# Optimization experiments

Measured on AMD Instinct MI355X. Metric: run time of the kernel, lower is better.

Reference implementation:

```python
import jax, jax.numpy as jnp
from jax import lax
import numpy as np

B, L, C, PRED = 64, 512, 321, 96
PATCH, STRIDE = 16, 8
N = (L - PATCH) // STRIDE + 1 + 1  # 64 patches (after replication pad)
HID = PATCH * 2                    # expansion_factor=2
ALPHA, EPS = 0.2, 1e-5

def gelu(v):
    return jax.nn.gelu(v, approximate=False)  # torch nn.GELU default (erf)

def setup_inputs() -> dict:
    key = jax.random.key(0)
    ks = jax.random.split(key, 10)
    init = lambda k, s: (jax.random.normal(k, s) * 0.02).astype(jnp.float32)
    return dict(
        x=jax.random.normal(ks[0], (B, L, C), jnp.float32),
        rev_w=jnp.ones((C,), jnp.float32), rev_b=jnp.zeros((C,), jnp.float32),
        fc1_w=init(ks[1], (HID, PATCH)), fc1_b=jnp.zeros((HID,), jnp.float32),
        bn1_w=jnp.ones((N,), jnp.float32), bn1_b=jnp.zeros((N,), jnp.float32),
        conv_w=init(ks[2], (N, 1, 3)), conv_b=jnp.zeros((N,), jnp.float32),
        bn2_w=jnp.ones((N,), jnp.float32), bn2_b=jnp.zeros((N,), jnp.float32),
        fc2_w=init(ks[3], (PATCH, HID)), fc2_b=jnp.zeros((PATCH,), jnp.float32),
        m1_w=init(ks[4], (2 * N, N)), m1_b=jnp.zeros((2 * N,), jnp.float32),
        m2_w=init(ks[5], (N, 2 * N)), m2_b=jnp.zeros((N,), jnp.float32),
        gl_scale=jnp.full((1,), 0.1, jnp.float32),
        ln_w=jnp.ones((PATCH,), jnp.float32), ln_b=jnp.zeros((PATCH,), jnp.float32),
        seas_w=init(ks[6], (PRED, N * PATCH)), seas_b=jnp.zeros((PRED,), jnp.float32),
        tr_w=init(ks[7], (PRED, L)), tr_b=jnp.zeros((PRED,), jnp.float32),
        fus_w=init(ks[8], (PRED, 2 * PRED)), fus_b=jnp.zeros((PRED,), jnp.float32),
    )

def _batchnorm(h, w, b):
    # BatchNorm1d over channel axis N (train-mode batch stats, biased var)
    mu = h.mean((0, 2), keepdims=True)
    var = h.var((0, 2), keepdims=True)
    return (h - mu) * lax.rsqrt(var + EPS) * w[None, :, None] + b[None, :, None]

def reference(x, rev_w, rev_b, fc1_w, fc1_b, bn1_w, bn1_b, conv_w, conv_b,
              bn2_w, bn2_b, fc2_w, fc2_b, m1_w, m1_b, m2_w, m2_b, gl_scale,
              ln_w, ln_b, seas_w, seas_b, tr_w, tr_b, fus_w, fus_b):
    # --- RevIN norm (torch std is unbiased, ddof=1) ---
    mean = x.mean(1, keepdims=True)
    std = jnp.std(x, axis=1, ddof=1, keepdims=True) + EPS
    xn = (x - mean) / std * rev_w + rev_b
    # --- EMA trend/seasonal decomposition via scan ---
    xt = jnp.moveaxis(xn, 1, 0)                      # [L,B,C]
    def step(c, xi):
        t = ALPHA * xi + (1.0 - ALPHA) * c
        return t, t
    _, rest = lax.scan(step, xt[0], xt[1:])
    trend = jnp.moveaxis(jnp.concatenate([xt[:1], rest], 0), 0, 1)  # [B,L,C]
    seasonal = xn - trend
    # --- patching (replication pad right by STRIDE, unfold) ---
    s = seasonal.transpose(0, 2, 1).reshape(B * C, L)
    s = jnp.concatenate([s, jnp.broadcast_to(s[:, -1:], (B * C, STRIDE))], axis=1)
    idx = np.arange(N)[:, None] * STRIDE + np.arange(PATCH)[None, :]
    sp = s[:, idx]                                    # [B*C, N, PATCH]
    # --- IntraPatch (local): fc1 -> GELU -> BN -> depthwise conv -> GELU -> BN -> fc2 + res ---
    h = gelu(sp @ fc1_w.T + fc1_b)                    # [BC,N,HID]
    h = _batchnorm(h, bn1_w, bn1_b)
    h = lax.conv_general_dilated(h, conv_w, (1,), ((1, 1),),
                                 feature_group_count=N,
                                 dimension_numbers=('NCH', 'OIH', 'NCH'))
    h = h + conv_b[None, :, None]
    h = _batchnorm(gelu(h), bn2_w, bn2_b)
    local = h @ fc2_w.T + fc2_b + sp                  # dropout is identity (eval)
    # --- InterPatch (global): pool -> MLP -> sigmoid gate ---
    pooled = sp.mean(-1)                              # [BC,N]
    w = jax.nn.sigmoid(gelu(pooled @ m1_w.T + m1_b) @ m2_w.T + m2_b)
    glob = sp * (1.0 + gl_scale * w[..., None])
    # --- fusion 'add' + residual LayerNorm over PATCH ---
    y = sp + local + glob
    mu = y.mean(-1, keepdims=True)
    var = y.var(-1, keepdims=True)
    y = (y - mu) * lax.rsqrt(var + EPS) * ln_w + ln_b
    # --- heads ---
    s_pred = y.reshape(B * C, N * PATCH) @ seas_w.T + seas_b
    t = trend.transpose(0, 2, 1).reshape(B * C, L)
    t_pred = t @ tr_w.T + tr_b
    out = jnp.concatenate([s_pred, t_pred], -1) @ fus_w.T + fus_b
    out = out.reshape(B, C, PRED).transpose(0, 2, 1)  # [B,PRED,C]
    # --- RevIN denorm ---
    out = (out - rev_b) / rev_w
    return out * std + mean
```

## Files before the change

### kernel.cpp

```cpp
#include <hip/hip_runtime.h>
#include <hip/hip_bf16.h>
#include <math.h>

#define B_    64
#define L_    512
#define C_    321
#define PRED_ 96
#define N_    64
#define HID_  32
#define BC_   (B_*C_)
#define SROW_ 528
#define EPS_  1e-5f
#define ALPHA_ 0.2f
#define GR_   16
#define RB_   8
#define NBLK2_ (BC_/GR_)
#define NBLKH_ (BC_/8)
#define D64_  6.2771017353866808e-7f
#define STW_  548
#define UTW_  260

typedef __attribute__((ext_vector_type(8))) short bf16x8;
typedef __attribute__((ext_vector_type(4))) float f32x4;

__device__ __forceinline__ float gelu_f(float x){
  float ax = fabsf(x);
  float z  = ax * 0.70710678118654752440f;
  float t  = __builtin_amdgcn_rcpf(fmaf(0.3275911f, z, 1.0f));
  float poly = fmaf(fmaf(fmaf(fmaf(1.061405429f, t, -1.453152027f),
                   t, 1.421413741f), t, -0.284496736f), t, 0.254829592f) * t;
  float e  = __expf(-z*z);
  float erfp = fmaf(-poly, e, 1.0f);
  return fmaf(0.5f*ax, erfp, 0.5f*x);
}
__device__ __forceinline__ unsigned short bf16bits(float x){
  __hip_bfloat16 h = __float2bfloat16(x);
  return *(unsigned short*)&h;
}

__global__ __launch_bounds__(256) void k1_all(
    const float* __restrict__ x, const float* __restrict__ rev_w, const float* __restrict__ rev_b,
    const float* __restrict__ seas_w, const float* __restrict__ tr_w, const float* __restrict__ fus_w,
    const float* __restrict__ seas_b, const float* __restrict__ tr_b, const float* __restrict__ fus_b,
    float* __restrict__ s_raw, __hip_bfloat16* __restrict__ t_bf, float* __restrict__ rowpar,
    float* __restrict__ pooled,
    __hip_bfloat16* __restrict__ Wsf, __hip_bfloat16* __restrict__ Wtf,
    float* __restrict__ biasc, float* __restrict__ colsumT) {
  __shared__ float lf[8][32];
  __shared__ float psum[8][32], psq[8][32];
  __shared__ float fs[8][32];
  __shared__ float st[32*STW_];
  int tid = threadIdx.x;
  int bid = blockIdx.x;
  if (bid >= BC_/32) {
    int fb = bid - BC_/32;
    if (fb < 576) {
      int idx = fb*256 + tid;
      int j = idx / 1536, k = idx - j*1536;
      float acc = 0.f;
      if (k < 1024) {
        for (int i=0;i<96;++i) acc = fmaf(fus_w[j*192+i], seas_w[i*1024+k], acc);
        Wsf[(size_t)j*1024 + k] = __float2bfloat16(acc);
      } else {
        int l = k - 1024;
        for (int i=0;i<96;++i) acc = fmaf(fus_w[j*192+96+i], tr_w[i*512+l], acc);
        Wtf[(size_t)j*512 + l] = __float2bfloat16(acc);
      }
    } else {
      __shared__ float rowsum[96];
      if (tid < 96) {
        float s = 0.f;
        for (int l=0;l<512;++l) s += tr_w[tid*512+l];
        rowsum[tid] = s;
      }
      __syncthreads();
      if (tid < 96) {
        float acc = fus_b[tid], cs = 0.f;
        for (int i=0;i<96;++i) {
          acc = fmaf(fus_w[tid*192+i],    seas_b[i], acc);
          acc = fmaf(fus_w[tid*192+96+i], tr_b[i],   acc);
          cs  = fmaf(fus_w[tid*192+96+i], rowsum[i], cs);
        }
        biasc[tid] = acc; colsumT[tid] = cs;
      }
    }
    return;
  }
  int q = tid >> 5, r = tid & 31;
  int row0 = bid*32;
  int row = row0 + r;
  int b = row / C_, c = row - b*C_;
  const float* xp = x + (size_t)b*L_*C_ + c;
  int l0 = q*64;
  float sreg[64];
  float loc = 0.f, sum = 0.f, sq = 0.f;
  #pragma unroll
  for (int i=0;i<64;++i) {
    float v = xp[(size_t)(l0+i)*C_];
    sum += v; sq = fmaf(v,v,sq);
    loc = (q==0 && i==0) ? v : fmaf(ALPHA_, v, 0.8f*loc);
    sreg[i] = loc;
  }
  lf[q][r] = loc; psum[q][r] = sum; psq[q][r] = sq;
  __syncthreads();
  float cin = 0.f;
  for (int j=0;j<q;++j) cin = fmaf(D64_, cin, lf[j][r]);
  float S=0.f, Q=0.f;
  #pragma unroll
  for (int qq=0;qq<8;++qq){ S += psum[qq][r]; Q += psq[qq][r]; }
  float mean = S*(1.0f/512.0f);
  float var  = (Q - S*S*(1.0f/512.0f))*(1.0f/511.0f);
  var = fmaxf(var, 0.f);
  float stdv = sqrtf(var) + EPS_;
  float rwc = rev_w[c];
  float a = rwc / stdv;
  if (q==0) {
    float rbc = rev_b[c];
    float g = rbc - mean*a;
    float inva = stdv / rwc;
    ((float4*)rowpar)[row] = make_float4(a, g, mean, inva);
  }
  float prev = 0.f, f = 1.f, slast = 0.f;
  float sums8[8];
  #pragma unroll
  for (int j=0;j<8;++j) sums8[j] = 0.f;
  #pragma unroll
  for (int i=0;i<64;++i) {
    float lc = sreg[i];
    f *= 0.8f;
    float s = (q==0 && i==0) ? 0.f : fmaf(4.f, lc - prev, -f*cin);
    prev = lc;
    float sv = s * a;
    st[r*STW_ + q*64 + i] = sv;
    sums8[i>>3] += sv;
    slast = sv;
  }
  fs[q][r] = sums8[0];
  if (q==7) {
    #pragma unroll
    for (int k=0;k<8;++k) st[r*STW_ + 512 + k] = slast;
  }
  __syncthreads();
  for (int idx=tid; idx<32*130; idx+=256) {
    int rr = idx/130, g = idx - rr*130;
    float4 v = *(float4*)&st[rr*STW_ + g*4];
    *(float4*)&s_raw[(size_t)(row0+rr)*SROW_ + g*4] = v;
  }
  {
    float nf = (q < 7) ? fs[q+1][r] : 8.0f*slast;
    #pragma unroll
    for (int j=0;j<7;++j)
      pooled[(size_t)row*64 + q*8 + j] = (sums8[j] + sums8[j+1])*(1.0f/16.0f);
    pooled[(size_t)row*64 + q*8 + 7] = (sums8[7] + nf)*(1.0f/16.0f);
  }
  __syncthreads();
  unsigned* tb = (unsigned*)st;
  {
    float f2 = 1.f; unsigned lo = 0;
    #pragma unroll
    for (int i=0;i<64;++i) {
      f2 *= 0.8f;
      float tt = fmaf(f2, cin, sreg[i]) * a;
      unsigned hb = bf16bits(tt);
      if ((i&1)==0) lo = hb;
      else tb[r*UTW_ + q*32 + (i>>1)] = lo | (hb<<16);
    }
  }
  __syncthreads();
  for (int idx=tid; idx<32*64; idx+=256) {
    int rr = idx>>6, g = idx&63;
    uint4 v = *(uint4*)&tb[rr*UTW_ + g*4];
    *(uint4*)&t_bf[(size_t)(row0+rr)*512 + g*8] = v;
  }
}

__global__ __launch_bounds__(512) void k4_gate(
    const float* __restrict__ pooled,
    const float* __restrict__ m1_w, const float* __restrict__ m1_b,
    const float* __restrict__ m2_w, const float* __restrict__ m2_b,
    float* __restrict__ wl_g) {
  __shared__ __align__(16) __hip_bfloat16 buf[17408];
  int t = threadIdx.x;
  int row0 = blockIdx.x*64;
  __hip_bfloat16* A1 = buf;
  __hip_bfloat16* B1 = buf + 4608;
  __hip_bfloat16* H1 = buf;
  __hip_bfloat16* B2 = buf + 8704;
  for (int idx=t; idx<4096; idx+=512) {
    int r = idx>>6, k = idx&63;
    A1[r*72+k] = __float2bfloat16(pooled[(size_t)(row0+r)*64 + k]);
  }
  for (int idx=t; idx<8192; idx+=512) {
    int r = idx>>6, k = idx&63;
    B1[r*72+k] = __float2bfloat16(m1_w[idx]);
  }
  __syncthreads();
  int lane = t & 63, w = t >> 6;
  int fr = lane & 15, fg = lane >> 4;
  int mt = w & 3;
  int ng0 = (w>>2)*4;
  f32x4 acc1[4];
  #pragma unroll
  for (int nn=0;nn<4;++nn) acc1[nn] = (f32x4){0.f,0.f,0.f,0.f};
  #pragma unroll
  for (int ksub=0; ksub<2; ++ksub) {
    bf16x8 av = *(bf16x8*)&A1[(mt*16+fr)*72 + ksub*32 + fg*8];
    #pragma unroll
    for (int nn=0;nn<4;++nn) {
      bf16x8 bv = *(bf16x8*)&B1[((ng0+nn)*16+fr)*72 + ksub*32 + fg*8];
      acc1[nn] = __builtin_amdgcn_mfma_f32_16x16x32_bf16(av, bv, acc1[nn], 0,0,0);
    }
  }
  __syncthreads();
  #pragma unroll
  for (int nn=0;nn<4;++nn) {
    int col = (ng0+nn)*16 + fr;
    float bias = m1_b[col];
    #pragma unroll
    for (int reg=0;reg<4;++reg) {
      int row = mt*16 + fg*4 + reg;
      H1[row*136 + col] = __float2bfloat16(gelu_f(acc1[nn][reg] + bias));
    }
  }
  for (int idx=t; idx<8192; idx+=512) {
    int r = idx>>7, k = idx&127;
    B2[r*136+k] = __float2bfloat16(m2_w[idx]);
  }
  __syncthreads();
  int nt0 = (w>>2)*2;
  f32x4 acc2[2];
  #pragma unroll
  for (int nn=0;nn<2;++nn) acc2[nn] = (f32x4){0.f,0.f,0.f,0.f};
  #pragma unroll
  for (int ksub=0; ksub<4; ++ksub) {
    bf16x8 av = *(bf16x8*)&H1[(mt*16+fr)*136 + ksub*32 + fg*8];
    #pragma unroll
    for (int nn=0;nn<2;++nn) {
      bf16x8 bv = *(bf16x8*)&B2[((nt0+nn)*16+fr)*136 + ksub*32 + fg*8];
      acc2[nn] = __builtin_amdgcn_mfma_f32_16x16x32_bf16(av, bv, acc2[nn], 0,0,0);
    }
  }
  #pragma unroll
  for (int nn=0;nn<2;++nn) {
    int col = (nt0+nn)*16 + fr;
    float bias = m2_b[col];
    #pragma unroll
    for (int reg=0;reg<4;++reg) {
      int row = mt*16 + fg*4 + reg;
      wl_g[(size_t)(row0+row)*64 + col] = 1.0f/(1.0f + __expf(-(acc2[nn][reg] + bias)));
    }
  }
}

__global__ __launch_bounds__(256) void k2_bn1stats(
    const float* __restrict__ s_raw,
    const float* __restrict__ fc1_w, const float* __restrict__ fc1_b,
    float* __restrict__ partials) {
  __shared__ float sl[GR_*SROW_];
  __shared__ float red[2][GR_*64];
  int t = threadIdx.x;
  int row0 = blockIdx.x*GR_;
  for (int idx=t; idx<GR_*520; idx+=256) {
    int rr = idx/520, cc = idx - rr*520;
    sl[rr*SROW_+cc] = s_raw[(size_t)(row0+rr)*SROW_+cc];
  }
  __syncthreads();
  int lr = t >> 4, ng = t & 15;
  for (int q=0;q<4;++q) {
    int n = ng + 16*q;
    float sp[16];
    #pragma unroll
    for (int p=0;p<16;++p) sp[p] = sl[lr*SROW_ + n*8 + p];
    float s1=0.f, s2=0.f;
    #pragma unroll
    for (int hid=0; hid<32; ++hid) {
      float acc = fc1_b[hid];
      #pragma unroll
      for (int p=0;p<16;++p) acc = fmaf(sp[p], fc1_w[hid*16+p], acc);
      float gv = gelu_f(acc);
      s1 += gv; s2 = fmaf(gv,gv,s2);
    }
    red[0][lr*64+n] = s1;
    red[1][lr*64+n] = s2;
  }
  __syncthreads();
  if (t < 64) {
    float S1=0.f, S2=0.f;
    for (int lr2=0; lr2<GR_; ++lr2) { S1 += red[0][lr2*64+t]; S2 += red[1][lr2*64+t]; }
    partials[((size_t)blockIdx.x*64+t)*2+0] = S1;
    partials[((size_t)blockIdx.x*64+t)*2+1] = S2;
  }
}

__global__ __launch_bounds__(512) void k2v2_bn1_cr(
    const float* __restrict__ s_raw,
    const float* __restrict__ fc1_w, const float* __restrict__ fc1_b,
    const float* __restrict__ conv_w,
    float* __restrict__ partials, __hip_bfloat16* __restrict__ crp) {
  __shared__ float cw[192];
  __shared__ float red[2][512];
  int t = threadIdx.x;
  int row0 = blockIdx.x*8;
  if (t < 192) cw[t] = conv_w[t];
  __syncthreads();
  int lr = t>>6, n = t&63;
  const float* sp_g = &s_raw[(size_t)(row0+lr)*SROW_ + n*8];
  float sp[16];
  {
    float4 v0 = *(const float4*)(sp_g);
    float4 v1 = *(const float4*)(sp_g+4);
    float4 v2 = *(const float4*)(sp_g+8);
    float4 v3 = *(const float4*)(sp_g+12);
    sp[0]=v0.x; sp[1]=v0.y; sp[2]=v0.z; sp[3]=v0.w;
    sp[4]=v1.x; sp[5]=v1.y; sp[6]=v1.z; sp[7]=v1.w;
    sp[8]=v2.x; sp[9]=v2.y; sp[10]=v2.z; sp[11]=v2.w;
    sp[12]=v3.x; sp[13]=v3.y; sp[14]=v3.z; sp[15]=v3.w;
  }
  float w0=cw[n*3], wm=cw[n*3+1], wp=cw[n*3+2];
  float s1=0.f, s2=0.f;
  auto gf = [&](int k)->float {
    float acc = fc1_b[k];
    #pragma unroll
    for (int p=0;p<16;++p) acc = fmaf(sp[p], fc1_w[k*16+p], acc);
    float g = gelu_f(acc);
    s1 += g; s2 = fmaf(g,g,s2);
    return g;
  };
  float gm = 0.f, gc = gf(0), gp = gf(1);
  unsigned wds[16]; unsigned crlo = 0;
  #pragma unroll
  for (int k=0;k<32;++k) {
    float cr = fmaf(gm, w0, fmaf(gc, wm, (k<31) ? gp*wp : 0.f));
    unsigned hb = bf16bits(cr);
    if ((k&1)==0) crlo = hb; else wds[k>>1] = crlo | (hb<<16);
    gm = gc; gc = gp;
    gp = (k+2<32) ? gf(k+2) : 0.f;
  }
  uint4* dst = (uint4*)&crp[((size_t)(row0+lr)*64 + n)*32];
  dst[0] = make_uint4(wds[0],wds[1],wds[2],wds[3]);
  dst[1] = make_uint4(wds[4],wds[5],wds[6],wds[7]);
  dst[2] = make_uint4(wds[8],wds[9],wds[10],wds[11]);
  dst[3] = make_uint4(wds[12],wds[13],wds[14],wds[15]);
  red[0][t] = s1;
  red[1][t] = s2;
  __syncthreads();
  if (t < 64) {
    float S1=0.f, S2=0.f;
    #pragma unroll
    for (int lr2=0; lr2<8; ++lr2) { S1 += red[0][lr2*64+t]; S2 += red[1][lr2*64+t]; }
    partials[((size_t)blockIdx.x*64+t)*2+0] = S1;
    partials[((size_t)blockIdx.x*64+t)*2+1] = S2;
  }
}

__global__ __launch_bounds__(256) void k_bnreduce(
    const float* __restrict__ partials, int nblk,
    const float* __restrict__ bnw, const float* __restrict__ bnb,
    float* __restrict__ scale, float* __restrict__ shift) {
  __shared__ float red[2][256];
  int n = blockIdx.x, t = threadIdx.x;
  float s1=0.f, s2=0.f;
  for (int i=t; i<nblk; i+=256) {
    s1 += partials[((size_t)i*64+n)*2+0];
    s2 += partials[((size_t)i*64+n)*2+1];
  }
  red[0][t]=s1; red[1][t]=s2;
  __syncthreads();
  for (int off=128; off>0; off>>=1) {
    if (t<off) { red[0][t]+=red[0][t+off]; red[1][t]+=red[1][t+off]; }
    __syncthreads();
  }
  if (t==0) {
    const float count = (float)BC_ * 32.0f;
    float mu = red[0][0]/count;
    float var = red[1][0]/count - mu*mu;
    float sc = rsqrtf(var + EPS_) * bnw[n];
    scale[n] = sc;
    shift[n] = bnb[n] - mu*sc;
  }
}

__global__ __launch_bounds__(256) void k3_bn2stats(
    const float* __restrict__ s_raw,
    const float* __restrict__ fc1_w, const float* __restrict__ fc1_b,
    const float* __restrict__ scale1, const float* __restrict__ shift1,
    const float* __restrict__ conv_w, const float* __restrict__ conv_b,
    float* __restrict__ partials) {
  __shared__ float sl[GR_*SROW_];
  __shared__ float sc1[64], sh1[64], cw[192], cb[64];
  __shared__ float red[2][GR_*64];
  int t = threadIdx.x;
  int row0 = blockIdx.x*GR_;
  if (t < 64) { sc1[t]=scale1[t]; sh1[t]=shift1[t]; cb[t]=conv_b[t]; }
  if (t >= 64 && t < 256) cw[t-64] = conv_w[t-64];
  __syncthreads();
  for (int idx=t; idx<GR_*520; idx+=256) {
    int rr = idx/520, cc = idx - rr*520;
    sl[rr*SROW_+cc] = s_raw[(size_t)(row0+rr)*SROW_+cc];
  }
  __syncthreads();
  int lr = t >> 4, ng = t & 15;
  for (int q=0;q<4;++q) {
    int n = ng + 16*q;
    float sp[16];
    #pragma unroll
    for (int p=0;p<16;++p) sp[p] = sl[lr*SROW_ + n*8 + p];
    float scn = sc1[n], shn = sh1[n];
    float h[32];
    #pragma unroll
    for (int hid=0; hid<32; ++hid) {
      float acc = fc1_b[hid];
      #pragma unroll
      for (int p=0;p<16;++p) acc = fmaf(sp[p], fc1_w[hid*16+p], acc);
      h[hid] = fmaf(gelu_f(acc), scn, shn);
    }
    float w0=cw[n*3], wm=cw[n*3+1], wpp=cw[n*3+2], cbn=cb[n];
    float s1=0.f, s2=0.f, prev=0.f;
    #pragma unroll
    for (int k2=0;k2<32;++k2) {
      float cur = h[k2];
      float cv = cbn;
      cv = fmaf(prev, w0, cv);
      cv = fmaf(cur, wm, cv);
      if (k2<31) cv = fmaf(h[k2+1], wpp, cv);
      float gv = gelu_f(cv);
      s1 += gv; s2 = fmaf(gv,gv,s2);
      prev = cur;
    }
    red[0][lr*64+n]=s1; red[1][lr*64+n]=s2;
  }
  __syncthreads();
  if (t < 64) {
    float S1=0.f, S2=0.f;
    for (int lr2=0; lr2<GR_; ++lr2) { S1 += red[0][lr2*64+t]; S2 += red[1][lr2*64+t]; }
    partials[((size_t)blockIdx.x*64+t)*2+0] = S1;
    partials[((size_t)blockIdx.x*64+t)*2+1] = S2;
  }
}

__global__ __launch_bounds__(512) void k3v2_bn2stats(
    __hip_bfloat16* __restrict__ crp,
    const float* __restrict__ scale1, const float* __restrict__ shift1,
    const float* __restrict__ conv_w, const float* __restrict__ conv_b,
    float* __restrict__ partials) {
  __shared__ float sc1[64], sh0l[64], shml[64], sh31l[64];
  __shared__ float red[2][512];
  int t = threadIdx.x;
  int row0 = blockIdx.x*8;
  if (t < 64) {
    float w0=conv_w[t*3], wm=conv_w[t*3+1], wp=conv_w[t*3+2];
    float s1v=shift1[t], cbv=conv_b[t];
    sc1[t]  = scale1[t];
    sh0l[t] = fmaf(s1v, wm+wp, cbv);
    shml[t] = fmaf(s1v, w0+wm+wp, cbv);
    sh31l[t]= fmaf(s1v, w0+wm, cbv);
  }
  __syncthreads();
  int lr = t>>6, n = t&63;
  uint4* crb = (uint4*)&crp[((size_t)(row0+lr)*64 + n)*32];
  uint4 u0=crb[0], u1=crb[1], u2=crb[2], u3=crb[3];
  unsigned uw[16] = {u0.x,u0.y,u0.z,u0.w, u1.x,u1.y,u1.z,u1.w,
                     u2.x,u2.y,u2.z,u2.w, u3.x,u3.y,u3.z,u3.w};
  float sc1n = sc1[n];
  float shm = shml[n];
  float s1=0.f, s2=0.f;
  unsigned wds[16];
  #pragma unroll
  for (int j=0;j<16;++j) {
    unsigned u = uw[j];
    float c0 = __uint_as_float(u<<16);
    float c1 = __uint_as_float(u & 0xffff0000u);
    float sh_0 = (j==0)  ? sh0l[n]  : shm;
    float sh_1 = (j==15) ? sh31l[n] : shm;
    float g0 = gelu_f(fmaf(c0, sc1n, sh_0));
    float g1 = gelu_f(fmaf(c1, sc1n, sh_1));
    s1 += g0 + g1;
    s2 = fmaf(g0,g0, fmaf(g1,g1, s2));
    wds[j] = (unsigned)bf16bits(g0) | (((unsigned)bf16bits(g1))<<16);
  }
  crb[0] = make_uint4(wds[0],wds[1],wds[2],wds[3]);
  crb[1] = make_uint4(wds[4],wds[5],wds[6],wds[7]);
  crb[2] = make_uint4(wds[8],wds[9],wds[10],wds[11]);
  crb[3] = make_uint4(wds[12],wds[13],wds[14],wds[15]);
  red[0][t]=s1; red[1][t]=s2;
  __syncthreads();
  if (t < 64) {
    float S1=0.f, S2=0.f;
    #pragma unroll
    for (int lr2=0; lr2<8; ++lr2) { S1 += red[0][lr2*64+t]; S2 += red[1][lr2*64+t]; }
    partials[((size_t)blockIdx.x*64+t)*2+0] = S1;
    partials[((size_t)blockIdx.x*64+t)*2+1] = S2;
  }
}

__global__ __launch_bounds__(256) void k5a_pipeline(
    const float* __restrict__ s_raw, const float* __restrict__ wl_g,
    const float* __restrict__ fc1_w, const float* __restrict__ fc1_b,
    const float* __restrict__ scale1, const float* __restrict__ shift1,
    const float* __restrict__ conv_w, const float* __restrict__ conv_b,
    const float* __restrict__ scale2, const float* __restrict__ shift2,
    const float* __restrict__ fc2_w, const float* __restrict__ fc2_b,
    const float* __restrict__ gl_scale,
    const float* __restrict__ ln_w, const float* __restrict__ ln_b,
    __hip_bfloat16* __restrict__ ybf) {
  __shared__ float sl[RB_*SROW_];
  __shared__ float cw[192], cb[64];
  __shared__ float sc1[64], sh1[64], sc2[64], sh2[64];
  int t = threadIdx.x;
  int row0 = blockIdx.x*RB_;
  if (t<64) { sc1[t]=scale1[t]; sh1[t]=shift1[t]; sc2[t]=scale2[t]; sh2[t]=shift2[t]; cb[t]=conv_b[t]; }
  if (t>=64 && t<256) cw[t-64]=conv_w[t-64];
  __syncthreads();
  for (int idx=t; idx<RB_*520; idx+=256) {
    int rr = idx/520, cc = idx - rr*520;
    sl[rr*SROW_+cc] = s_raw[(size_t)(row0+rr)*SROW_+cc];
  }
  __syncthreads();
  float glv = gl_scale[0];
  for (int idx=t; idx<RB_*64; idx+=256) {
    int rr = idx>>6, n = idx&63;
    float wlv = wl_g[(size_t)row0*64 + idx];
    float h[32];
    {
      float sp[16];
      #pragma unroll
      for (int p=0;p<16;++p) sp[p] = sl[rr*SROW_ + n*8 + p];
      float scn=sc1[n], shn=sh1[n];
      #pragma unroll
      for (int hid=0;hid<32;++hid) {
        float acc=fc1_b[hid];
        #pragma unroll
        for (int p=0;p<16;++p) acc=fmaf(sp[p], fc1_w[hid*16+p], acc);
        h[hid]=fmaf(gelu_f(acc), scn, shn);
      }
    }
    {
      float w0=cw[n*3], wm=cw[n*3+1], wpp=cw[n*3+2], cbn=cb[n];
      float sc2n=sc2[n], sh2n=sh2[n];
      float prev=0.f;
      #pragma unroll
      for (int k2=0;k2<32;++k2) {
        float cur = h[k2];
        float cv = cbn;
        cv = fmaf(prev, w0, cv);
        cv = fmaf(cur, wm, cv);
        if (k2<31) cv = fmaf(h[k2+1], wpp, cv);
        h[k2] = fmaf(gelu_f(cv), sc2n, sh2n);
        prev = cur;
      }
    }
    float yv[16];
    #pragma unroll
    for (int p=0;p<16;++p) {
      float acc=fc2_b[p];
      #pragma unroll
      for (int hid=0;hid<32;++hid) acc=fmaf(h[hid], fc2_w[p*32+hid], acc);
      yv[p]=acc;
    }
    float smul = 3.0f + glv*wlv;
    float mu=0.f;
    #pragma unroll
    for (int p=0;p<16;++p) {
      yv[p]=fmaf(sl[rr*SROW_ + n*8 + p], smul, yv[p]);
      mu+=yv[p];
    }
    mu *= (1.0f/16.0f);
    float var=0.f;
    #pragma unroll
    for (int p=0;p<16;++p){ float d=yv[p]-mu; var=fmaf(d,d,var); }
    var *= (1.0f/16.0f);
    float rs = rsqrtf(var + EPS_);
    unsigned int wds[8];
    #pragma unroll
    for (int j=0;j<8;++j) {
      unsigned int lo = bf16bits(fmaf((yv[2*j]-mu)*rs,   ln_w[2*j],   ln_b[2*j]));
      unsigned int hi = bf16bits(fmaf((yv[2*j+1]-mu)*rs, ln_w[2*j+1], ln_b[2*j+1]));
      wds[j] = lo | (hi<<16);
    }
    size_t ybase = (size_t)(row0+rr)*1024 + n*16;
    uint4* dst = (uint4*)&ybf[ybase];
    dst[0] = make_uint4(wds[0],wds[1],wds[2],wds[3]);
    dst[1] = make_uint4(wds[4],wds[5],wds[6],wds[7]);
  }
}

__global__ __launch_bounds__(512) void k5a_v3(
    const float* __restrict__ s_raw, const float* __restrict__ wl_g,
    const __hip_bfloat16* __restrict__ g2p,
    const float* __restrict__ scale2, const float* __restrict__ shift2,
    const float* __restrict__ fc2_w, const float* __restrict__ fc2_b,
    const float* __restrict__ gl_scale,
    const float* __restrict__ ln_w, const float* __restrict__ ln_b,
    __hip_bfloat16* __restrict__ ybf) {
  __shared__ float sc2[64], sh2[64];
  int t = threadIdx.x;
  int row0 = blockIdx.x*RB_;
  if (t < 64) { sc2[t]=scale2[t]; sh2[t]=shift2[t]; }
  __syncthreads();
  int rr = t>>6, n = t&63;
  int row = row0 + rr;
  float glv = gl_scale[0];
  float wlv = wl_g[(size_t)row*64 + n];
  const uint4* crb = (const uint4*)&g2p[((size_t)row*64 + n)*32];
  uint4 u0=crb[0], u1=crb[1], u2=crb[2], u3=crb[3];
  unsigned uw[16] = {u0.x,u0.y,u0.z,u0.w, u1.x,u1.y,u1.z,u1.w,
                     u2.x,u2.y,u2.z,u2.w, u3.x,u3.y,u3.z,u3.w};
  float sc2n = sc2[n], sh2n = sh2[n];
  float yv[16];
  #pragma unroll
  for (int p=0;p<16;++p) yv[p] = fc2_b[p];
  #pragma unroll
  for (int j=0;j<16;++j) {
    unsigned u = uw[j];
    int k0 = 2*j, k1 = 2*j+1;
    float g0 = __uint_as_float(u<<16);
    float g1 = __uint_as_float(u & 0xffff0000u);
    float h2a = fmaf(g0, sc2n, sh2n);
    float h2b = fmaf(g1, sc2n, sh2n);
    #pragma unroll
    for (int p=0;p<16;++p)
      yv[p] = fmaf(h2a, fc2_w[p*32+k0], fmaf(h2b, fc2_w[p*32+k1], yv[p]));
  }
  const float* sp_g = &s_raw[(size_t)row*SROW_ + n*8];
  float4 s0 = *(const float4*)(sp_g);
  float4 s1v = *(const float4*)(sp_g+4);
  float4 s2v = *(const float4*)(sp_g+8);
  float4 s3 = *(const float4*)(sp_g+12);
  float sp[16] = {s0.x,s0.y,s0.z,s0.w, s1v.x,s1v.y,s1v.z,s1v.w,
                  s2v.x,s2v.y,s2v.z,s2v.w, s3.x,s3.y,s3.z,s3.w};
  float smul = 3.0f + glv*wlv;
  float mu=0.f;
  #pragma unroll
  for (int p=0;p<16;++p) {
    yv[p] = fmaf(sp[p], smul, yv[p]);
    mu += yv[p];
  }
  mu *= (1.0f/16.0f);
  float var=0.f;
  #pragma unroll
  for (int p=0;p<16;++p){ float d=yv[p]-mu; var=fmaf(d,d,var); }
  var *= (1.0f/16.0f);
  float rs = rsqrtf(var + EPS_);
  unsigned int wds[8];
  #pragma unroll
  for (int j=0;j<8;++j) {
    unsigned int lo = bf16bits(fmaf((yv[2*j]-mu)*rs,   ln_w[2*j],   ln_b[2*j]));
    unsigned int hi = bf16bits(fmaf((yv[2*j+1]-mu)*rs, ln_w[2*j+1], ln_b[2*j+1]));
    wds[j] = lo | (hi<<16);
  }
  size_t ybase = (size_t)row*1024 + n*16;
  uint4* dst = (uint4*)&ybf[ybase];
  dst[0] = make_uint4(wds[0],wds[1],wds[2],wds[3]);
  dst[1] = make_uint4(wds[4],wds[5],wds[6],wds[7]);
}

__global__ __launch_bounds__(384) void k5b_gemm(
    const __hip_bfloat16* __restrict__ ybf, const __hip_bfloat16* __restrict__ tbf,
    const __hip_bfloat16* __restrict__ Wsf, const __hip_bfloat16* __restrict__ Wtf,
    const float* __restrict__ rowpar, const float* __restrict__ rev_b,
    const float* __restrict__ biasc, const float* __restrict__ colsumT,
    float* __restrict__ out) {
  __shared__ __align__(16) __hip_bfloat16 As[2*16*72];
  __shared__ __align__(16) __hip_bfloat16 Bs[2*96*72];
  __shared__ float rp[64];
  __shared__ float rbl[16];
  __shared__ int   obase[16];
  __shared__ float bcl[96], csl[96];
  int tid = threadIdx.x;
  int row0 = blockIdx.x*16;
  if (tid < 64) rp[tid] = rowpar[(size_t)row0*4 + tid];
  if (tid >= 64 && tid < 80) {
    int lr = tid-64;
    int row = row0 + lr; int b = row/C_; int c = row - b*C_;
    rbl[lr] = rev_b[c]; obase[lr] = b*PRED_*C_ + c;
  }
  if (tid >= 96 && tid < 192) { bcl[tid-96]=biasc[tid-96]; csl[tid-96]=colsumT[tid-96]; }
  int lane = tid & 63, w = tid >> 6;
  int fr = lane & 15, fg = lane >> 4;
  bool a0 = tid < 128;
  int r0 = a0 ? (tid>>3) : ((tid-128)>>3);
  int c0 = a0 ? (tid&7)  : ((tid-128)&7);
  int r1 = (tid+256)>>3, c1 = (tid+256)&7;
  bool h2 = tid < 128;
  int r2 = (tid+640)>>3, c2 = (tid+640)&7;
  f32x4 acc = (f32x4){0.f,0.f,0.f,0.f};

  uint4 v0, v1, v2;
  auto LOAD = [&](int ks){
    const __hip_bfloat16* Ag; const __hip_bfloat16* Bg; int K; int kofs;
    if (ks < 8) { Ag = tbf + (size_t)row0*512;  Bg = Wtf; K = 512;  kofs = ks*64; }
    else        { Ag = ybf + (size_t)row0*1024; Bg = Wsf; K = 1024; kofs = (ks-8)*64; }
    v0 = a0 ? *(const uint4*)(Ag + (size_t)r0*K + kofs + c0*8)
            : *(const uint4*)(Bg + (size_t)r0*K + kofs + c0*8);
    v1 = *(const uint4*)(Bg + (size_t)r1*K + kofs + c1*8);
    if (h2) v2 = *(const uint4*)(Bg + (size_t)r2*K + kofs + c2*8);
  };

  LOAD(0);
  int cur = 0;
  for (int ks=0; ks<24; ++ks) {
    __hip_bfloat16* Ab = &As[cur*16*72];
    __hip_bfloat16* Bb = &Bs[cur*96*72];
    if (a0) *(uint4*)&Ab[r0*72 + c0*8] = v0;
    else    *(uint4*)&Bb[r0*72 + c0*8] = v0;
    *(uint4*)&Bb[r1*72 + c1*8] = v1;
    if (h2) *(uint4*)&Bb[r2*72 + c2*8] = v2;
    __syncthreads();
    if (ks < 23) LOAD(ks+1);
    #pragma unroll
    for (int ksub=0; ksub<2; ++ksub) {
      bf16x8 av = *(bf16x8*)&Ab[fr*72 + ksub*32 + fg*8];
      bf16x8 bv = *(bf16x8*)&Bb[(w*16+fr)*72 + ksub*32 + fg*8];
      acc = __builtin_amdgcn_mfma_f32_16x16x32_bf16(av, bv, acc, 0,0,0);
    }
    cur ^= 1;
  }
  {
    int col = w*16 + fr;
    float cs = csl[col], bc = bcl[col];
    #pragma unroll
    for (int reg=0;reg<4;++reg) {
      int rloc = fg*4 + reg;
      float g = rp[rloc*4+1], meanv = rp[rloc*4+2], inva = rp[rloc*4+3];
      float val = acc[reg] + g*cs + bc;
      val = (val - rbl[rloc])*inva + meanv;
      out[(size_t)obase[rloc] + (size_t)col*C_] = val;
    }
  }
}

extern "C" void kernel_launch(void* const* d_in, const int* in_sizes, int n_in,
                              void* d_out, int out_size, void* d_ws, size_t ws_size,
                              hipStream_t stream) {
  const float* x      = (const float*)d_in[0];
  const float* rev_w  = (const float*)d_in[1];
  const float* rev_b  = (const float*)d_in[2];
  const float* fc1_w  = (const float*)d_in[3];
  const float* fc1_b  = (const float*)d_in[4];
  const float* bn1_w  = (const float*)d_in[5];
  const float* bn1_b  = (const float*)d_in[6];
  const float* conv_w = (const float*)d_in[7];
  const float* conv_b = (const float*)d_in[8];
  const float* bn2_w  = (const float*)d_in[9];
  const float* bn2_b  = (const float*)d_in[10];
  const float* fc2_w  = (const float*)d_in[11];
  const float* fc2_b  = (const float*)d_in[12];
  const float* m1_w   = (const float*)d_in[13];
  const float* m1_b   = (const float*)d_in[14];
  const float* m2_w   = (const float*)d_in[15];
  const float* m2_b   = (const float*)d_in[16];
  const float* gl     = (const float*)d_in[17];
  const float* ln_w   = (const float*)d_in[18];
  const float* ln_b   = (const float*)d_in[19];
  const float* seas_w = (const float*)d_in[20];
  const float* seas_b = (const float*)d_in[21];
  const float* tr_w   = (const float*)d_in[22];
  const float* tr_b   = (const float*)d_in[23];
  const float* fus_w  = (const float*)d_in[24];
  const float* fus_b  = (const float*)d_in[25];
  float* out = (float*)d_out;
  float* ws = (float*)d_ws;

  __hip_bfloat16* Wsf  = (__hip_bfloat16*)(ws);
  __hip_bfloat16* Wtf  = (__hip_bfloat16*)(ws + 49152);
  float* biasc   = ws + 73728;
  float* colsumT = ws + 73856;
  float* scale1  = ws + 73984;
  float* shift1  = ws + 74048;
  float* scale2  = ws + 74112;
  float* shift2  = ws + 74176;
  float* partials= ws + 74240;
  float* rowpar  = ws + 238592;
  float* s_raw   = ws + 320768;
  __hip_bfloat16* t_bf = (__hip_bfloat16*)(ws + 11168000);
  __hip_bfloat16* ybf  = (__hip_bfloat16*)(ws + 16427264);
  float* pooled  = ws + 26945792;
  float* wl_g    = ws + 28260608;
  __hip_bfloat16* crp  = (__hip_bfloat16*)(ws + 29575424);
  float* pbig    = ws + 16427264;
  const size_t NEED = (29575424ull + 21037056ull) * 4ull;
  bool big = (ws_size >= NEED);

  hipLaunchKernelGGL(k1_all, dim3(BC_/32 + 577), dim3(256), 0, stream,
    x, rev_w, rev_b, seas_w, tr_w, fus_w, seas_b, tr_b, fus_b,
    s_raw, t_bf, rowpar, pooled, Wsf, Wtf, biasc, colsumT);
  hipLaunchKernelGGL(k4_gate, dim3(BC_/64), dim3(512), 0, stream, pooled, m1_w, m1_b, m2_w, m2_b, wl_g);
  if (big) {
    hipLaunchKernelGGL(k2v2_bn1_cr, dim3(NBLKH_), dim3(512), 0, stream, s_raw, fc1_w, fc1_b, conv_w, pbig, crp);
    hipLaunchKernelGGL(k_bnreduce, dim3(64), dim3(256), 0, stream, pbig, NBLKH_, bn1_w, bn1_b, scale1, shift1);
    hipLaunchKernelGGL(k3v2_bn2stats, dim3(NBLKH_), dim3(512), 0, stream, crp, scale1, shift1, conv_w, conv_b, pbig);
    hipLaunchKernelGGL(k_bnreduce, dim3(64), dim3(256), 0, stream, pbig, NBLKH_, bn2_w, bn2_b, scale2, shift2);
    hipLaunchKernelGGL(k5a_v3, dim3(NBLKH_), dim3(512), 0, stream,
      s_raw, wl_g, crp, scale2, shift2, fc2_w, fc2_b, gl, ln_w, ln_b, ybf);
  } else {
    hipLaunchKernelGGL(k2_bn1stats, dim3(NBLK2_), dim3(256), 0, stream, s_raw, fc1_w, fc1_b, partials);
    hipLaunchKernelGGL(k_bnreduce, dim3(64), dim3(256), 0, stream, partials, NBLK2_, bn1_w, bn1_b, scale1, shift1);
    hipLaunchKernelGGL(k3_bn2stats, dim3(NBLK2_), dim3(256), 0, stream, s_raw, fc1_w, fc1_b, scale1, shift1, conv_w, conv_b, partials);
    hipLaunchKernelGGL(k_bnreduce, dim3(64), dim3(256), 0, stream, partials, NBLK2_, bn2_w, bn2_b, scale2, shift2);
    hipLaunchKernelGGL(k5a_pipeline, dim3(BC_/RB_), dim3(256), 0, stream,
      s_raw, wl_g, fc1_w, fc1_b, scale1, shift1, conv_w, conv_b,
      scale2, shift2, fc2_w, fc2_b, gl, ln_w, ln_b, ybf);
  }
  hipLaunchKernelGGL(k5b_gemm, dim3(BC_/16), dim3(384), 0, stream,
    ybf, t_bf, Wsf, Wtf, rowpar, rev_b, biasc, colsumT, out);
}
```

Before: 211.3 us.

## Compute fc1 projection with bf16 MFMA in bn1/conv kernel

Replaces per-thread scalar fc1 dot products with a bf16 MFMA GEMM over the block's 512 patches. Inputs and weights are staged in LDS as bf16, and GELU outputs are written back to LDS in bf16 before the depthwise conv and BN1 statistics pass. This targets the scalar FMA cost. In exchange it adds LDS traffic, extra barriers, larger shared memory use that may cut occupancy, and bf16 rounding of the hidden activations before stats.

```diff
diff --git a/kernel.cpp b/kernel.cpp
--- a/kernel.cpp
+++ b/kernel.cpp
@@ -292,57 +292,102 @@
   }
 }
 
-__global__ __launch_bounds__(512) void k2v2_bn1_cr(
+__global__ __launch_bounds__(512) void k2v3_bn1_cr(
     const float* __restrict__ s_raw,
     const float* __restrict__ fc1_w, const float* __restrict__ fc1_b,
     const float* __restrict__ conv_w,
     float* __restrict__ partials, __hip_bfloat16* __restrict__ crp) {
+  __shared__ __align__(16) __hip_bfloat16 Ab[512*24];
+  __shared__ __align__(16) __hip_bfloat16 Bb[32*24];
+  __shared__ __align__(16) __hip_bfloat16 Hb[512*40];
   __shared__ float cw[192];
   __shared__ float red[2][512];
   int t = threadIdx.x;
   int row0 = blockIdx.x*8;
   if (t < 192) cw[t] = conv_w[t];
-  __syncthreads();
-  int lr = t>>6, n = t&63;
-  const float* sp_g = &s_raw[(size_t)(row0+lr)*SROW_ + n*8];
-  float sp[16];
   {
+    int hid = t>>4, k = t&15;
+    if (t < 512) Bb[hid*24+k] = __float2bfloat16(fc1_w[hid*16+k]);
+  }
+  {
+    int lr = t>>6, n = t&63;
+    const float* sp_g = &s_raw[(size_t)(row0+lr)*SROW_ + n*8];
     float4 v0 = *(const float4*)(sp_g);
     float4 v1 = *(const float4*)(sp_g+4);
     float4 v2 = *(const float4*)(sp_g+8);
     float4 v3 = *(const float4*)(sp_g+12);
-    sp[0]=v0.x; sp[1]=v0.y; sp[2]=v0.z; sp[3]=v0.w;
-    sp[4]=v1.x; sp[5]=v1.y; sp[6]=v1.z; sp[7]=v1.w;
-    sp[8]=v2.x; sp[9]=v2.y; sp[10]=v2.z; sp[11]=v2.w;
-    sp[12]=v3.x; sp[13]=v3.y; sp[14]=v3.z; sp[15]=v3.w;
-  }
-  float w0=cw[n*3], wm=cw[n*3+1], wp=cw[n*3+2];
-  float s1=0.f, s2=0.f;
-  auto gf = [&](int k)->float {
-    float acc = fc1_b[k];
-    #pragma unroll
-    for (int p=0;p<16;++p) acc = fmaf(sp[p], fc1_w[k*16+p], acc);
-    float g = gelu_f(acc);
-    s1 += g; s2 = fmaf(g,g,s2);
-    return g;
-  };
-  float gm = 0.f, gc = gf(0), gp = gf(1);
-  unsigned wds[16]; unsigned crlo = 0;
-  #pragma unroll
-  for (int k=0;k<32;++k) {
-    float cr = fmaf(gm, w0, fmaf(gc, wm, (k<31) ? gp*wp : 0.f));
-    unsigned hb = bf16bits(cr);
-    if ((k&1)==0) crlo = hb; else wds[k>>1] = crlo | (hb<<16);
-    gm = gc; gc = gp;
-    gp = (k+2<32) ? gf(k+2) : 0.f;
-  }
-  uint4* dst = (uint4*)&crp[((size_t)(row0+lr)*64 + n)*32];
-  dst[0] = make_uint4(wds[0],wds[1],wds[2],wds[3]);
-  dst[1] = make_uint4(wds[4],wds[5],wds[6],wds[7]);
-  dst[2] = make_uint4(wds[8],wds[9],wds[10],wds[11]);
-  dst[3] = make_uint4(wds[12],wds[13],wds[14],wds[15]);
-  red[0][t] = s1;
-  red[1][t] = s2;
+    float sp[16] = {v0.x,v0.y,v0.z,v0.w, v1.x,v1.y,v1.z,v1.w,
+                    v2.x,v2.y,v2.z,v2.w, v3.x,v3.y,v3.z,v3.w};
+    #pragma unroll
+    for (int k=0;k<16;++k) Ab[t*24+k] = __float2bfloat16(sp[k]);
+  }
+  __syncthreads();
+  int lane = t & 63, w = t >> 6;
+  int fr = lane & 15, fg = lane >> 4;
+  bf16x8 z8 = (bf16x8){0,0,0,0,0,0,0,0};
+  f32x4 acc[4][2];
+  #pragma unroll
+  for (int mt=0;mt<4;++mt)
+    #pragma unroll
+    for (int nt=0;nt<2;++nt) acc[mt][nt] = (f32x4){0.f,0.f,0.f,0.f};
+  #pragma unroll
+  for (int mt=0;mt<4;++mt) {
+    int mrow = (w*4+mt)*16 + fr;
+    bf16x8 av = (fg < 2) ? *(bf16x8*)&Ab[mrow*24 + fg*8] : z8;
+    #pragma unroll
+    for (int nt=0;nt<2;++nt) {
+      bf16x8 bv = (fg < 2) ? *(bf16x8*)&Bb[(nt*16+fr)*24 + fg*8] : z8;
+      acc[mt][nt] = __builtin_amdgcn_mfma_f32_16x16x32_bf16(av, bv, acc[mt][nt], 0,0,0);
+    }
+  }
+  __syncthreads();
+  #pragma unroll
+  for (int mt=0;mt<4;++mt) {
+    #pragma unroll
+    for (int nt=0;nt<2;++nt) {
+      int hid = nt*16 + fr;
+      float bias = fc1_b[hid];
+      #pragma unroll
+      for (int reg=0;reg<4;++reg) {
+        int p = (w*4+mt)*16 + fg*4 + reg;
+        Hb[p*40 + hid] = __float2bfloat16(gelu_f(acc[mt][nt][reg] + bias));
+      }
+    }
+  }
+  __syncthreads();
+  {
+    int n = t & 63;
+    const uint4* hb = (const uint4*)&Hb[t*40];
+    uint4 u0=hb[0], u1=hb[1], u2=hb[2], u3=hb[3];
+    unsigned uw[16] = {u0.x,u0.y,u0.z,u0.w, u1.x,u1.y,u1.z,u1.w,
+                       u2.x,u2.y,u2.z,u2.w, u3.x,u3.y,u3.z,u3.w};
+    float g[32];
+    #pragma unroll
+    for (int j=0;j<16;++j) {
+      g[2*j]   = __uint_as_float(uw[j]<<16);
+      g[2*j+1] = __uint_as_float(uw[j] & 0xffff0000u);
+    }
+    float s1=0.f, s2=0.f;
+    #pragma unroll
+    for (int k=0;k<32;++k) { s1 += g[k]; s2 = fmaf(g[k], g[k], s2); }
+    float w0=cw[n*3], wm=cw[n*3+1], wp=cw[n*3+2];
+    unsigned wds[16]; unsigned crlo = 0;
+    float prevv = 0.f;
+    #pragma unroll
+    for (int k=0;k<32;++k) {
+      float cr = fmaf(prevv, w0, fmaf(g[k], wm, (k<31) ? g[k+1]*wp : 0.f));
+      prevv = g[k];
+      unsigned hbits = bf16bits(cr);
+      if ((k&1)==0) crlo = hbits; else wds[k>>1] = crlo | (hbits<<16);
+    }
+    uint4* dst = (uint4*)&crp[((size_t)row0*64 + t)*32];
+    dst[0] = make_uint4(wds[0],wds[1],wds[2],wds[3]);
+    dst[1] = make_uint4(wds[4],wds[5],wds[6],wds[7]);
+    dst[2] = make_uint4(wds[8],wds[9],wds[10],wds[11]);
+    dst[3] = make_uint4(wds[12],wds[13],wds[14],wds[15]);
+    red[0][t] = s1;
+    red[1][t] = s2;
+  }
   __syncthreads();
   if (t < 64) {
     float S1=0.f, S2=0.f;
@@ -786,7 +831,7 @@
     s_raw, t_bf, rowpar, pooled, Wsf, Wtf, biasc, colsumT);
   hipLaunchKernelGGL(k4_gate, dim3(BC_/64), dim3(512), 0, stream, pooled, m1_w, m1_b, m2_w, m2_b, wl_g);
   if (big) {
-    hipLaunchKernelGGL(k2v2_bn1_cr, dim3(NBLKH_), dim3(512), 0, stream, s_raw, fc1_w, fc1_b, conv_w, pbig, crp);
+    hipLaunchKernelGGL(k2v3_bn1_cr, dim3(NBLKH_), dim3(512), 0, stream, s_raw, fc1_w, fc1_b, conv_w, pbig, crp);
     hipLaunchKernelGGL(k_bnreduce, dim3(64), dim3(256), 0, stream, pbig, NBLKH_, bn1_w, bn1_b, scale1, shift1);
     hipLaunchKernelGGL(k3v2_bn2stats, dim3(NBLKH_), dim3(512), 0, stream, crp, scale1, shift1, conv_w, conv_b, pbig);
     hipLaunchKernelGGL(k_bnreduce, dim3(64), dim3(256), 0, stream, pbig, NBLKH_, bn2_w, bn2_b, scale2, shift2);
```

Result: no change. 212.3 us (+0.5%).
